# Kernel optimization log

Hardware: AMD Instinct MI355X
Metric: run time of the kernel (lower is better)

## Reference

```python
import jax, jax.numpy as jnp
import numpy as np

N_NODES = 20000
N_EDGES = 320000
X_DIM = 128
EDGE_DIM = 64
HIDDEN = 256
OUT_DIM = 256
LAYERS = 3
N_GRAPHS = 64


def setup_inputs() -> dict:
    key = jax.random.key(0)
    ks = jax.random.split(key, 20)
    x = jax.random.normal(ks[0], (N_NODES, X_DIM), dtype=jnp.float32)
    edge_index = jax.random.randint(ks[1], (2, N_EDGES), 0, N_NODES, dtype=jnp.int64)
    edge_attr = jax.random.normal(ks[2], (N_EDGES, EDGE_DIM), dtype=jnp.float32)
    batch_ids = jnp.sort(jax.random.randint(ks[3], (N_NODES,), 0, N_GRAPHS, dtype=jnp.int64))

    def lin(k, fan_in, fan_out):
        bound = 1.0 / np.sqrt(fan_in)
        kw, kb = jax.random.split(k)
        W = jax.random.uniform(kw, (fan_in, fan_out), minval=-bound, maxval=bound, dtype=jnp.float32)
        b = jax.random.uniform(kb, (fan_out,), minval=-bound, maxval=bound, dtype=jnp.float32)
        return W, b

    xproj_W, xproj_b = lin(ks[4], X_DIM, HIDDEN)
    edge_W, edge_b, mlp_W1, mlp_b1, mlp_W2, mlp_b2 = [], [], [], [], [], []
    for l in range(LAYERS):
        eW, eb = lin(ks[5 + l], EDGE_DIM, HIDDEN)
        w1, b1 = lin(ks[8 + l], HIDDEN, HIDDEN)
        w2, b2 = lin(ks[11 + l], HIDDEN, HIDDEN)
        edge_W.append(eW); edge_b.append(eb)
        mlp_W1.append(w1); mlp_b1.append(b1)
        mlp_W2.append(w2); mlp_b2.append(b2)
    out_W1, out_b1 = lin(ks[14], HIDDEN, HIDDEN)
    out_W2, out_b2 = lin(ks[15], HIDDEN, OUT_DIM)
    return {
        "x": x, "edge_index": edge_index, "edge_attr": edge_attr, "batch_ids": batch_ids,
        "xproj_W": xproj_W, "xproj_b": xproj_b,
        "edge_W": jnp.stack(edge_W), "edge_b": jnp.stack(edge_b),
        "mlp_W1": jnp.stack(mlp_W1), "mlp_b1": jnp.stack(mlp_b1),
        "mlp_W2": jnp.stack(mlp_W2), "mlp_b2": jnp.stack(mlp_b2),
        "out_W1": out_W1, "out_b1": out_b1, "out_W2": out_W2, "out_b2": out_b2,
    }


def reference(x, edge_index, edge_attr, batch_ids, xproj_W, xproj_b,
              edge_W, edge_b, mlp_W1, mlp_b1, mlp_W2, mlp_b2,
              out_W1, out_b1, out_W2, out_b2):
    src, dst = edge_index[0], edge_index[1]
    h = x @ xproj_W + xproj_b  # [N, H]
    for l in range(LAYERS):
        # GINE message: relu(x_j + Lin(edge_attr)), aggregated by sum at target
        msg = jax.nn.relu(h[src] + edge_attr @ edge_W[l] + edge_b[l])  # [E, H]
        agg = jax.ops.segment_sum(msg, dst, num_segments=N_NODES)      # [N, H]
        z = h + agg  # (1 + eps) * x_i with eps = 0
        z = jax.nn.relu(z @ mlp_W1[l] + mlp_b1[l]) @ mlp_W2[l] + mlp_b2[l]
        h = jax.nn.relu(z)  # outer F.relu in forward
    # global mean pool over graphs
    sums = jax.ops.segment_sum(h, batch_ids, num_segments=N_GRAPHS)    # [G, H]
    counts = jax.ops.segment_sum(jnp.ones((h.shape[0],), h.dtype), batch_ids, num_segments=N_GRAPHS)
    g = sums / jnp.maximum(counts, 1.0)[:, None]
    g = jax.nn.relu(g @ out_W1 + out_b1) @ out_W2 + out_b2
    # F.normalize(dim=-1): x / max(||x||_2, eps)
    norm = jnp.maximum(jnp.linalg.norm(g, axis=-1, keepdims=True), 1e-12)
    return g / norm
```

## Files before the change

### kernel.cpp

```cpp
#include <hip/hip_runtime.h>

#define N_NODES 20000
#define N_EDGES 320000
#define X_DIM 128
#define EDGE_DIM 64
#define HIDDEN 256
#define N_GRAPHS 64
#define LAYERS 3

#define NPB 8
#define EB 32
#define NB 16
#define PSPLIT 8
#define NBLK ((N_NODES + 255) / 256)

typedef __attribute__((ext_vector_type(8))) short short8;
typedef __attribute__((ext_vector_type(4))) float floatx4;

__device__ __forceinline__ unsigned short f2bf(float f) {
    union { float f; unsigned u; } v; v.f = f;
    return (unsigned short)((v.u + 0x7FFFu + ((v.u >> 16) & 1u)) >> 16);
}
__device__ __forceinline__ float bf2f(unsigned short u) {
    return __uint_as_float(((unsigned)u) << 16);
}


__global__ __launch_bounds__(256) void deg_kernel(const int* __restrict__ ei,
                                                  int* __restrict__ deg)
{
    int e = blockIdx.x * 256 + threadIdx.x;
    if (e < N_EDGES) atomicAdd(&deg[ei[N_EDGES + e]], 1);
}

__global__ __launch_bounds__(256) void pscan_kernel(const int* __restrict__ deg,
                                                    int* __restrict__ rp,
                                                    int* __restrict__ bsum)
{
    __shared__ int buf[256];
    const int t = threadIdx.x;
    const int i = blockIdx.x * 256 + t;
    int v = (i < N_NODES) ? deg[i] : 0;
    buf[t] = v;
    __syncthreads();
    for (int off = 1; off < 256; off <<= 1) {
        int a = (t >= off) ? buf[t - off] : 0;
        __syncthreads();
        buf[t] += a;
        __syncthreads();
    }
    if (i < N_NODES) rp[i] = buf[t] - v;
    if (t == 255) bsum[blockIdx.x] = buf[255];
}

__global__ __launch_bounds__(128) void bscan_kernel(const int* __restrict__ bsum,
                                                    int* __restrict__ boff)
{
    __shared__ int buf[128];
    const int t = threadIdx.x;
    int v = (t < NBLK) ? bsum[t] : 0;
    buf[t] = v;
    __syncthreads();
    for (int off = 1; off < 128; off <<= 1) {
        int a = (t >= off) ? buf[t - off] : 0;
        __syncthreads();
        buf[t] += a;
        __syncthreads();
    }
    if (t < NBLK) boff[t] = buf[t] - v;
}

__global__ __launch_bounds__(256) void addoff_kernel(int* __restrict__ rp,
                                                     const int* __restrict__ boff)
{
    const int i = blockIdx.x * 256 + threadIdx.x;
    if (i < N_NODES) rp[i] += boff[blockIdx.x];
    if (i == 0) rp[N_NODES] = N_EDGES;
}

__global__ __launch_bounds__(256) void scatter_kernel(const int* __restrict__ ei,
                                                      const int* __restrict__ rp,
                                                      int* __restrict__ cursor,
                                                      int* __restrict__ perm)
{
    const int e = blockIdx.x * 256 + threadIdx.x;
    if (e < N_EDGES) {
        const int d = ei[N_EDGES + e];
        const int pos = atomicAdd(&cursor[d], 1);
        perm[rp[d] + pos] = e;
    }
}

__global__ __launch_bounds__(256) void permute_kernel(
    const float* __restrict__ ea, const int* __restrict__ ei,
    const int* __restrict__ perm, unsigned short* __restrict__ eab,
    int* __restrict__ srcs, int* __restrict__ dsts)
{
    const int tid = blockIdx.x * 256 + threadIdx.x;
    const int e = tid >> 3, seg = tid & 7;
    const int p = perm[e];
    const float* sp = ea + (size_t)p * EDGE_DIM + seg * 8;
    const float4 v0 = *(const float4*)sp;
    const float4 v1 = *(const float4*)(sp + 4);
    short8 o;
    o[0] = (short)f2bf(v0.x); o[1] = (short)f2bf(v0.y);
    o[2] = (short)f2bf(v0.z); o[3] = (short)f2bf(v0.w);
    o[4] = (short)f2bf(v1.x); o[5] = (short)f2bf(v1.y);
    o[6] = (short)f2bf(v1.z); o[7] = (short)f2bf(v1.w);
    *(short8*)(eab + (size_t)e * EDGE_DIM + seg * 8) = o;
    if (seg == 0) { srcs[e] = ei[p]; dsts[e] = ei[N_EDGES + p]; }
}

__global__ __launch_bounds__(256) void swizzle_kernel(const float* __restrict__ W,
                                                      unsigned short* __restrict__ out,
                                                      int KK, int total)
{
    const int gi = blockIdx.x * 256 + threadIdx.x;
    if (gi >= total) return;
    const int per = 8192 * KK;
    const int l = gi / per, i = gi % per;
    const int j = i & 7, lane = (i >> 3) & 63, rem = i >> 9;
    const int kk = rem % KK, rem2 = rem / KK, nt = rem2 & 3, wvv = rem2 >> 2;
    const int n = wvv * 64 + nt * 16 + (lane & 15);
    const int k = kk * 32 + (lane >> 4) * 8 + j;
    out[(size_t)l * per + i] = f2bf(W[(size_t)l * per + k * HIDDEN + n]);
}


__global__ __launch_bounds__(256) void node_proj_kernel(
    const float* __restrict__ x, const float* __restrict__ W,
    const float* __restrict__ b, float* __restrict__ h,
    unsigned short* __restrict__ hbf)
{
    const int t = threadIdx.x;
    const int row0 = blockIdx.x * NPB;
    __shared__ float xs[NPB][X_DIM];
    for (int idx = t; idx < NPB * X_DIM; idx += 256)
        xs[idx / X_DIM][idx % X_DIM] = x[(size_t)row0 * X_DIM + idx];
    __syncthreads();
    float acc[NPB];
    const float bt = b[t];
#pragma unroll
    for (int r = 0; r < NPB; r++) acc[r] = bt;
    for (int k = 0; k < X_DIM; k++) {
        const float wv = W[k * HIDDEN + t];
#pragma unroll
        for (int r = 0; r < NPB; r++) acc[r] += xs[r][k] * wv;
    }
#pragma unroll
    for (int r = 0; r < NPB; r++) {
        const size_t idx = (size_t)(row0 + r) * HIDDEN + t;
        h[idx] = acc[r];
        hbf[idx] = f2bf(acc[r]);
    }
}

__global__ __launch_bounds__(256, 5) void edge_mfma_kernel(
    const unsigned short* __restrict__ eab, const int* __restrict__ srcs,
    const int* __restrict__ dsts, const int* __restrict__ rowptr,
    const unsigned short* __restrict__ Ws, const float* __restrict__ b,
    const unsigned short* __restrict__ hbf, const float* __restrict__ h,
    unsigned short* __restrict__ Abf)
{
    const int t = threadIdx.x;
    const int lane = t & 63, wv = t >> 6, q = lane >> 4, m15 = lane & 15;
    const int row0 = blockIdx.x * NB;

    __shared__ unsigned short msg[EB][260];

    const int e_start = rowptr[row0];
    const int e_end   = rowptr[row0 + NB];
    const int cnt = e_end - e_start;

    if (cnt == 0) {
#pragma unroll
        for (int r = 0; r < NB; r++)
            Abf[(size_t)(row0 + r) * HIDDEN + t] = f2bf(h[(size_t)(row0 + r) * HIDDEN + t]);
        return;
    }

    short8 bfr[4][2];
#pragma unroll
    for (int nt = 0; nt < 4; nt++)
#pragma unroll
        for (int kk = 0; kk < 2; kk++)
            bfr[nt][kk] = *(const short8*)(Ws + ((((wv * 4 + nt) * 2 + kk) * 64) + lane) * 8);
    float bv[4];
#pragma unroll
    for (int nt = 0; nt < 4; nt++) bv[nt] = b[wv * 64 + nt * 16 + m15];

    const int ntiles = (cnt + EB - 1) >> 5;
    int prev = dsts[e_start];
    for (int r = row0; r < prev; r++)
        Abf[(size_t)r * HIDDEN + t] = f2bf(h[(size_t)r * HIDDEN + t]);
    float s = 0.f;
    float hcur = h[(size_t)prev * HIDDEN + t];

    for (int tile = 0; tile < ntiles; tile++) {
        const int ebase = e_start + tile * EB;
        const int nin = min(EB, e_end - ebase);

        short8 a0[2], a1[2];
#pragma unroll
        for (int kk = 0; kk < 2; kk++) {
            a0[kk] = *(const short8*)(eab + (size_t)(ebase + m15) * EDGE_DIM + kk * 32 + q * 8);
            a1[kk] = *(const short8*)(eab + (size_t)(ebase + 16 + m15) * EDGE_DIM + kk * 32 + q * 8);
        }

#pragma unroll
        for (int mt = 0; mt < 2; mt++) {
            floatx4 acc[4];
#pragma unroll
            for (int nt = 0; nt < 4; nt++)
                acc[nt] = (floatx4){bv[nt], bv[nt], bv[nt], bv[nt]};
#pragma unroll
            for (int kk = 0; kk < 2; kk++) {
                const short8 a = mt ? a1[kk] : a0[kk];
#pragma unroll
                for (int nt = 0; nt < 4; nt++)
                    acc[nt] = __builtin_amdgcn_mfma_f32_16x16x32_bf16(a, bfr[nt][kk], acc[nt], 0, 0, 0);
            }
#pragma unroll
            for (int nt = 0; nt < 4; nt++)
#pragma unroll
                for (int r = 0; r < 4; r++)
                    msg[mt * 16 + q * 4 + r][wv * 64 + nt * 16 + m15] = f2bf(acc[nt][r]);
        }

        unsigned short hv[EB];
#pragma unroll
        for (int e = 0; e < EB; e++) {
            const int se = srcs[min(ebase + e, N_EDGES - 1)];
            hv[e] = hbf[(size_t)se * HIDDEN + t];
        }

#pragma unroll
        for (int e = 0; e < EB; e++) {
            if (e < nin) {
                const int d = dsts[min(ebase + e, N_EDGES - 1)];
                if (d != prev) {
                    Abf[(size_t)prev * HIDDEN + t] = f2bf(hcur + s);
                    for (int r = prev + 1; r < d; r++)
                        Abf[(size_t)r * HIDDEN + t] = f2bf(h[(size_t)r * HIDDEN + t]);
                    hcur = h[(size_t)d * HIDDEN + t];
                    s = 0.f; prev = d;
                }
                const float m = bf2f(msg[e][t]) + bf2f(hv[e]);
                s += m > 0.f ? m : 0.f;
            }
        }
    }
    Abf[(size_t)prev * HIDDEN + t] = f2bf(hcur + s);
    for (int r = prev + 1; r < row0 + NB; r++)
        Abf[(size_t)r * HIDDEN + t] = f2bf(h[(size_t)r * HIDDEN + t]);
}

__global__ __launch_bounds__(256) void mlp_mfma_kernel(
    const unsigned short* __restrict__ W1s, const float* __restrict__ b1,
    const unsigned short* __restrict__ W2s, const float* __restrict__ b2,
    const unsigned short* __restrict__ Abf,
    float* __restrict__ h, unsigned short* __restrict__ hbf)
{
    const int t = threadIdx.x;
    const int lane = t & 63, wv = t >> 6, q = lane >> 4, m15 = lane & 15;
    const int row0 = blockIdx.x * 32;
    __shared__ __align__(16) unsigned short zs[32][264];

    const size_t base = (size_t)row0 * HIDDEN;
#pragma unroll
    for (int i = 0; i < 4; i++) {
        const int idx = i * 256 + t;
        const int row = idx >> 5, col = idx & 31;
        *(short8*)&zs[row][col * 8] = *(const short8*)(Abf + base + (size_t)idx * 8);
    }
    __syncthreads();

    float b1v[4], b2v[4];
#pragma unroll
    for (int nt = 0; nt < 4; nt++) {
        const int c = wv * 64 + nt * 16 + m15;
        b1v[nt] = b1[c]; b2v[nt] = b2[c];
    }

    floatx4 acc[2][4];
#pragma unroll
    for (int mt = 0; mt < 2; mt++)
#pragma unroll
        for (int nt = 0; nt < 4; nt++)
            acc[mt][nt] = (floatx4){0.f, 0.f, 0.f, 0.f};

#pragma unroll
    for (int kk = 0; kk < 8; kk++) {
        short8 bfr[4];
#pragma unroll
        for (int nt = 0; nt < 4; nt++)
            bfr[nt] = *(const short8*)(W1s + ((((wv * 4 + nt) * 8 + kk) * 64) + lane) * 8);
        const short8 a0 = *(const short8*)&zs[m15][kk * 32 + q * 8];
        const short8 a1 = *(const short8*)&zs[16 + m15][kk * 32 + q * 8];
#pragma unroll
        for (int nt = 0; nt < 4; nt++) {
            acc[0][nt] = __builtin_amdgcn_mfma_f32_16x16x32_bf16(a0, bfr[nt], acc[0][nt], 0, 0, 0);
            acc[1][nt] = __builtin_amdgcn_mfma_f32_16x16x32_bf16(a1, bfr[nt], acc[1][nt], 0, 0, 0);
        }
    }
    __syncthreads();
#pragma unroll
    for (int mt = 0; mt < 2; mt++)
#pragma unroll
        for (int nt = 0; nt < 4; nt++)
#pragma unroll
            for (int r = 0; r < 4; r++) {
                const int row = mt * 16 + q * 4 + r, c = wv * 64 + nt * 16 + m15;
                const float v = acc[mt][nt][r] + b1v[nt];
                zs[row][c] = f2bf(v > 0.f ? v : 0.f);
            }
    __syncthreads();

#pragma unroll
    for (int mt = 0; mt < 2; mt++)
#pragma unroll
        for (int nt = 0; nt < 4; nt++)
            acc[mt][nt] = (floatx4){0.f, 0.f, 0.f, 0.f};

#pragma unroll
    for (int kk = 0; kk < 8; kk++) {
        short8 bfr[4];
#pragma unroll
        for (int nt = 0; nt < 4; nt++)
            bfr[nt] = *(const short8*)(W2s + ((((wv * 4 + nt) * 8 + kk) * 64) + lane) * 8);
        const short8 a0 = *(const short8*)&zs[m15][kk * 32 + q * 8];
        const short8 a1 = *(const short8*)&zs[16 + m15][kk * 32 + q * 8];
#pragma unroll
        for (int nt = 0; nt < 4; nt++) {
            acc[0][nt] = __builtin_amdgcn_mfma_f32_16x16x32_bf16(a0, bfr[nt], acc[0][nt], 0, 0, 0);
            acc[1][nt] = __builtin_amdgcn_mfma_f32_16x16x32_bf16(a1, bfr[nt], acc[1][nt], 0, 0, 0);
        }
    }
#pragma unroll
    for (int mt = 0; mt < 2; mt++)
#pragma unroll
        for (int nt = 0; nt < 4; nt++)
#pragma unroll
            for (int r = 0; r < 4; r++) {
                const int row = mt * 16 + q * 4 + r, c = wv * 64 + nt * 16 + m15;
                float v = acc[mt][nt][r] + b2v[nt];
                v = v > 0.f ? v : 0.f;
                const size_t idx = (size_t)(row0 + row) * HIDDEN + c;
                h[idx] = v;
                hbf[idx] = f2bf(v);
            }
}

__global__ __launch_bounds__(256) void pool_kernel(
    const float* __restrict__ h, const int* __restrict__ bid,
    float* __restrict__ gsum)
{
    const int g = blockIdx.x / PSPLIT;
    const int part = blockIdx.x % PSPLIT;
    const int t = threadIdx.x;
    int lo = 0, hi = N_NODES;
    while (lo < hi) { int mid = (lo + hi) >> 1; if (bid[mid] < g) lo = mid + 1; else hi = mid; }
    const int start = lo;
    hi = N_NODES;
    while (lo < hi) { int mid = (lo + hi) >> 1; if (bid[mid] < g + 1) lo = mid + 1; else hi = mid; }
    const int end = lo;
    const int len = end - start;
    const int chunk = (len + PSPLIT - 1) / PSPLIT;
    const int s0 = start + part * chunk;
    const int s1 = min(s0 + chunk, end);
    if (s0 >= s1) return;
    float s = 0.f;
    for (int i = s0; i < s1; i++) s += h[(size_t)i * HIDDEN + t];
    atomicAdd(&gsum[g * HIDDEN + t], s);
}

__global__ __launch_bounds__(256) void head_kernel(
    const float* __restrict__ gsum, const int* __restrict__ bid,
    const float* __restrict__ W1, const float* __restrict__ b1,
    const float* __restrict__ W2, const float* __restrict__ b2,
    float* __restrict__ out)
{
    const int g = blockIdx.x;
    const int t = threadIdx.x;
    __shared__ float gs[HIDDEN];
    __shared__ float t1[HIDDEN];
    __shared__ float red[256];
    int lo = 0, hi = N_NODES;
    while (lo < hi) { int mid = (lo + hi) >> 1; if (bid[mid] < g) lo = mid + 1; else hi = mid; }
    const int start = lo;
    hi = N_NODES;
    while (lo < hi) { int mid = (lo + hi) >> 1; if (bid[mid] < g + 1) lo = mid + 1; else hi = mid; }
    float cnt = (float)(lo - start);
    cnt = cnt > 1.f ? cnt : 1.f;
    gs[t] = gsum[g * HIDDEN + t] / cnt;
    __syncthreads();
    float acc = b1[t];
    for (int k = 0; k < HIDDEN; k++) acc += gs[k] * W1[k * HIDDEN + t];
    t1[t] = acc > 0.f ? acc : 0.f;
    __syncthreads();
    float acc2 = b2[t];
    for (int k = 0; k < HIDDEN; k++) acc2 += t1[k] * W2[k * HIDDEN + t];
    red[t] = acc2 * acc2;
    __syncthreads();
    for (int s = 128; s > 0; s >>= 1) {
        if (t < s) red[t] += red[t + s];
        __syncthreads();
    }
    float norm = sqrtf(red[0]);
    norm = norm > 1e-12f ? norm : 1e-12f;
    out[g * HIDDEN + t] = acc2 / norm;
}

extern "C" void kernel_launch(void* const* d_in, const int* in_sizes, int n_in,
                              void* d_out, int out_size, void* d_ws, size_t ws_size,
                              hipStream_t stream)
{
    const float* x   = (const float*)d_in[0];
    const int*   ei  = (const int*)d_in[1];
    const float* ea  = (const float*)d_in[2];
    const int*   bid = (const int*)d_in[3];
    const float* xW  = (const float*)d_in[4];
    const float* xb  = (const float*)d_in[5];
    const float* eW  = (const float*)d_in[6];
    const float* eb  = (const float*)d_in[7];
    const float* W1  = (const float*)d_in[8];
    const float* b1  = (const float*)d_in[9];
    const float* W2  = (const float*)d_in[10];
    const float* b2  = (const float*)d_in[11];
    const float* oW1 = (const float*)d_in[12];
    const float* ob1 = (const float*)d_in[13];
    const float* oW2 = (const float*)d_in[14];
    const float* ob2 = (const float*)d_in[15];
    float* out = (float*)d_out;

    char* p = (char*)d_ws;
    auto alloc = [&](size_t bytes) { char* r = p; p += (bytes + 255) & ~(size_t)255; return r; };
    float* h     = (float*)alloc((size_t)N_NODES * HIDDEN * 4);
    float* gpool = (float*)alloc((size_t)N_GRAPHS * HIDDEN * 4);
    int* deg     = (int*)alloc(N_NODES * 4);
    int* rowptr  = (int*)alloc((N_NODES + 1) * 4);
    int* cursor  = (int*)alloc(N_NODES * 4);
    int* bsum    = (int*)alloc(NBLK * 4);
    int* boff    = (int*)alloc(NBLK * 4);
    int* perm    = (int*)alloc((size_t)N_EDGES * 4);
    int* srcs    = (int*)alloc((size_t)N_EDGES * 4);
    int* dsts    = (int*)alloc((size_t)N_EDGES * 4);
    unsigned short* hbf = (unsigned short*)alloc((size_t)N_NODES * HIDDEN * 2);
    unsigned short* Abf = (unsigned short*)alloc((size_t)N_NODES * HIDDEN * 2);
    unsigned short* eab = (unsigned short*)alloc((size_t)(N_EDGES + EB) * EDGE_DIM * 2);
    unsigned short* eWs = (unsigned short*)alloc((size_t)LAYERS * EDGE_DIM * HIDDEN * 2);
    unsigned short* W1s = (unsigned short*)alloc((size_t)LAYERS * HIDDEN * HIDDEN * 2);
    unsigned short* W2s = (unsigned short*)alloc((size_t)LAYERS * HIDDEN * HIDDEN * 2);

    hipMemsetAsync(deg, 0, N_NODES * sizeof(int), stream);
    hipMemsetAsync(cursor, 0, N_NODES * sizeof(int), stream);
    hipMemsetAsync(gpool, 0, N_GRAPHS * HIDDEN * sizeof(float), stream);
    deg_kernel<<<(N_EDGES + 255) / 256, 256, 0, stream>>>(ei, deg);
    pscan_kernel<<<NBLK, 256, 0, stream>>>(deg, rowptr, bsum);
    bscan_kernel<<<1, 128, 0, stream>>>(bsum, boff);
    addoff_kernel<<<NBLK, 256, 0, stream>>>(rowptr, boff);
    scatter_kernel<<<(N_EDGES + 255) / 256, 256, 0, stream>>>(ei, rowptr, cursor, perm);
    permute_kernel<<<(N_EDGES * 8) / 256, 256, 0, stream>>>(ea, ei, perm, eab, srcs, dsts);
    swizzle_kernel<<<(LAYERS * 8192 * 2 + 255) / 256, 256, 0, stream>>>(eW, eWs, 2, LAYERS * 8192 * 2);
    swizzle_kernel<<<(LAYERS * 8192 * 8 + 255) / 256, 256, 0, stream>>>(W1, W1s, 8, LAYERS * 8192 * 8);
    swizzle_kernel<<<(LAYERS * 8192 * 8 + 255) / 256, 256, 0, stream>>>(W2, W2s, 8, LAYERS * 8192 * 8);

    node_proj_kernel<<<N_NODES / NPB, 256, 0, stream>>>(x, xW, xb, h, hbf);
    for (int l = 0; l < LAYERS; l++) {
        edge_mfma_kernel<<<N_NODES / NB, 256, 0, stream>>>(
            eab, srcs, dsts, rowptr, eWs + (size_t)l * EDGE_DIM * HIDDEN,
            eb + l * HIDDEN, hbf, h, Abf);
        mlp_mfma_kernel<<<N_NODES / 32, 256, 0, stream>>>(
            W1s + (size_t)l * HIDDEN * HIDDEN, b1 + l * HIDDEN,
            W2s + (size_t)l * HIDDEN * HIDDEN, b2 + l * HIDDEN, Abf, h, hbf);
    }
    pool_kernel<<<N_GRAPHS * PSPLIT, 256, 0, stream>>>(h, bid, gpool);
    head_kernel<<<N_GRAPHS, 256, 0, stream>>>(gpool, bid, oW1, ob1, oW2, ob2, out);
}
```

Baseline: 626.1 us.

## Accumulate edge messages in a shared-memory buffer instead of run-length tracking

The branchy per-thread run-length aggregation over sorted destinations is replaced with a shared-memory float accumulator of NB rows. Each relu'd message is added with an LDS atomicAdd, and all rows are written out once at the end. The source-node gather is moved ahead of the MFMA edge projection so its load latency overlaps the matrix work. NB grows from 16 to 20, which divides the node count exactly, and the occupancy hint drops to 4 blocks per CU because of the extra LDS. The cost is more LDS per block and LDS atomics on every edge, though each thread only touches its own column.

```diff
diff --git a/kernel.cpp b/kernel.cpp
--- a/kernel.cpp
+++ b/kernel.cpp
@@ -10,7 +10,7 @@
 
 #define NPB 8
 #define EB 32
-#define NB 16
+#define NB 20
 #define PSPLIT 8
 #define NBLK ((N_NODES + 255) / 256)
 
@@ -155,7 +155,7 @@
     }
 }
 
-__global__ __launch_bounds__(256, 5) void edge_mfma_kernel(
+__global__ __launch_bounds__(256, 4) void edge_mfma_kernel(
     const unsigned short* __restrict__ eab, const int* __restrict__ srcs,
     const int* __restrict__ dsts, const int* __restrict__ rowptr,
     const unsigned short* __restrict__ Ws, const float* __restrict__ b,
@@ -167,17 +167,10 @@
     const int row0 = blockIdx.x * NB;
 
     __shared__ unsigned short msg[EB][260];
-
-    const int e_start = rowptr[row0];
-    const int e_end   = rowptr[row0 + NB];
-    const int cnt = e_end - e_start;
-
-    if (cnt == 0) {
-#pragma unroll
-        for (int r = 0; r < NB; r++)
-            Abf[(size_t)(row0 + r) * HIDDEN + t] = f2bf(h[(size_t)(row0 + r) * HIDDEN + t]);
-        return;
-    }
+    __shared__ float agg[NB][HIDDEN];
+
+#pragma unroll
+    for (int r = 0; r < NB; r++) agg[r][t] = 0.f;
 
     short8 bfr[4][2];
 #pragma unroll
@@ -189,12 +182,9 @@
 #pragma unroll
     for (int nt = 0; nt < 4; nt++) bv[nt] = b[wv * 64 + nt * 16 + m15];
 
-    const int ntiles = (cnt + EB - 1) >> 5;
-    int prev = dsts[e_start];
-    for (int r = row0; r < prev; r++)
-        Abf[(size_t)r * HIDDEN + t] = f2bf(h[(size_t)r * HIDDEN + t]);
-    float s = 0.f;
-    float hcur = h[(size_t)prev * HIDDEN + t];
+    const int e_start = rowptr[row0];
+    const int e_end   = rowptr[row0 + NB];
+    const int ntiles = (e_end - e_start + EB - 1) >> 5;
 
     for (int tile = 0; tile < ntiles; tile++) {
         const int ebase = e_start + tile * EB;
@@ -207,6 +197,13 @@
             a1[kk] = *(const short8*)(eab + (size_t)(ebase + 16 + m15) * EDGE_DIM + kk * 32 + q * 8);
         }
 
+        unsigned short hv[EB];
+#pragma unroll
+        for (int e = 0; e < EB; e++) {
+            const int se = srcs[min(ebase + e, N_EDGES - 1)];
+            hv[e] = hbf[(size_t)se * HIDDEN + t];
+        }
+
 #pragma unroll
         for (int mt = 0; mt < 2; mt++) {
             floatx4 acc[4];
@@ -227,32 +224,19 @@
                     msg[mt * 16 + q * 4 + r][wv * 64 + nt * 16 + m15] = f2bf(acc[nt][r]);
         }
 
-        unsigned short hv[EB];
-#pragma unroll
-        for (int e = 0; e < EB; e++) {
-            const int se = srcs[min(ebase + e, N_EDGES - 1)];
-            hv[e] = hbf[(size_t)se * HIDDEN + t];
-        }
-
 #pragma unroll
         for (int e = 0; e < EB; e++) {
             if (e < nin) {
-                const int d = dsts[min(ebase + e, N_EDGES - 1)];
-                if (d != prev) {
-                    Abf[(size_t)prev * HIDDEN + t] = f2bf(hcur + s);
-                    for (int r = prev + 1; r < d; r++)
-                        Abf[(size_t)r * HIDDEN + t] = f2bf(h[(size_t)r * HIDDEN + t]);
-                    hcur = h[(size_t)d * HIDDEN + t];
-                    s = 0.f; prev = d;
-                }
+                const int d = dsts[min(ebase + e, N_EDGES - 1)] - row0;
                 const float m = bf2f(msg[e][t]) + bf2f(hv[e]);
-                s += m > 0.f ? m : 0.f;
+                atomicAdd(&agg[d][t], m > 0.f ? m : 0.f);
             }
         }
     }
-    Abf[(size_t)prev * HIDDEN + t] = f2bf(hcur + s);
-    for (int r = prev + 1; r < row0 + NB; r++)
-        Abf[(size_t)r * HIDDEN + t] = f2bf(h[(size_t)r * HIDDEN + t]);
+
+#pragma unroll
+    for (int r = 0; r < NB; r++)
+        Abf[(size_t)(row0 + r) * HIDDEN + t] = f2bf(h[(size_t)(row0 + r) * HIDDEN + t] + agg[r][t]);
 }
 
 __global__ __launch_bounds__(256) void mlp_mfma_kernel(
```

Measured after the change: 1.751 ms. +179.7%, slower.
